# Kernel tuning notes

Measured on AMD Instinct MI355X. Metric: run time of the kernel, lower is better.

The kernel has to match this reference:

```python
import jax, jax.numpy as jnp
import numpy as np

C = 256
DQK = C // 8


def setup_inputs() -> dict:
    key = jax.random.key(0)
    ks = jax.random.split(key, 7)
    B, H, W = 8, 64, 64
    x = jax.random.normal(ks[0], (B, H, W, C), dtype=jnp.float32)
    # 1x1 conv weights (equivalent to per-pixel dense): [Cin, Cout] + bias
    sq = 1.0 / np.sqrt(C)
    Wq = jax.random.normal(ks[1], (C, DQK), dtype=jnp.float32) * sq
    bq = jnp.zeros((DQK,), dtype=jnp.float32)
    Wk = jax.random.normal(ks[2], (C, DQK), dtype=jnp.float32) * sq
    bk = jnp.zeros((DQK,), dtype=jnp.float32)
    Wv = jax.random.normal(ks[3], (C, C), dtype=jnp.float32) * sq
    bv = jnp.zeros((C,), dtype=jnp.float32)
    gamma = jnp.float32(0.5)  # nonzero so attention path affects output/grads
    return {"x": x, "Wq": Wq, "bq": bq, "Wk": Wk, "bk": bk,
            "Wv": Wv, "bv": bv, "gamma": gamma}


def reference(x, Wq, bq, Wk, bk, Wv, bv, gamma):
    B, H, W, c = x.shape
    n = H * W
    xf = x.reshape(B, n, c)                      # [B, hw, C]
    q = xf @ Wq + bq                              # [B, hw, C//8]
    k = xf @ Wk + bk                              # [B, hw, C//8]
    v = xf @ Wv + bv                              # [B, hw, C]
    scores = jnp.einsum('bnd,bmd->bnm', q, k)     # [B, hw, hw], no scaling (faithful)
    attn = jax.nn.softmax(scores, axis=-1)
    out = jnp.einsum('bnm,bmc->bnc', attn, v)     # [B, hw, C]
    out = out.reshape(B, H, W, c)
    return gamma * out + x
```

## Files before the change

kernel.cpp:

```cpp
#include <hip/hip_runtime.h>
#include <math.h>

#define B_ 8
#define N_ 4096
#define C_ 256
#define DQK_ 32

typedef float f32x4  __attribute__((ext_vector_type(4)));
typedef float f32x16 __attribute__((ext_vector_type(16)));
typedef short bf16x8 __attribute__((ext_vector_type(8)));
typedef short bf16x4 __attribute__((ext_vector_type(4)));

__device__ __forceinline__ short f2bf(float f){
  union { float f; unsigned u; } v; v.f = f;
  unsigned r = v.u + 0x7fffu + ((v.u >> 16) & 1u);
  return (short)(r >> 16);
}

__global__ void cast_wt_kernel(const float* __restrict__ Wq, const float* __restrict__ Wk,
                               const float* __restrict__ Wv, short* __restrict__ WT){
  int n = blockIdx.x;
  int k = threadIdx.x;
  float val;
  if (n < 32)       val = Wq[k*32 + n];
  else if (n < 64)  val = Wk[k*32 + (n-32)];
  else              val = Wv[k*256 + (n-64)];
  WT[n*256 + k] = f2bf(val);
}

__global__ __launch_bounds__(256) void proj_kernel(
    const float* __restrict__ x, const short* __restrict__ WT,
    const float* __restrict__ bq, const float* __restrict__ bk, const float* __restrict__ bv,
    short* __restrict__ qws, short* __restrict__ kws, short* __restrict__ vSw){
  __shared__ __align__(16) short sX[64*264];
  __shared__ __align__(16) short sT[64*72];
  int tid = threadIdx.x;
  int lane = tid & 63, wave = tid >> 6;
  int lane15 = lane & 15, quad = lane >> 4;
  int mbase = blockIdx.x * 64;
  int b = mbase >> 12, kvb = mbase & (N_-1);

  const float* xr = x + (size_t)mbase * C_;
  for (int i = 0; i < 8; i++){
    int s = tid + i*256;
    int row = s >> 5, cg = (s & 31) << 3;
    const f32x4* src = (const f32x4*)(xr + row*C_ + cg);
    f32x4 a = src[0], c = src[1];
    bf16x8 p;
    p[0]=f2bf(a[0]); p[1]=f2bf(a[1]); p[2]=f2bf(a[2]); p[3]=f2bf(a[3]);
    p[4]=f2bf(c[0]); p[5]=f2bf(c[1]); p[6]=f2bf(c[2]); p[7]=f2bf(c[3]);
    *(bf16x8*)(sX + row*264 + cg) = p;
  }
  __syncthreads();

  f32x4 acc[5][4];
  for (int i=0;i<5;i++) for (int mt=0;mt<4;mt++) acc[i][mt] = (f32x4)(0.f);

  for (int kc = 0; kc < 8; kc++){
    bf16x8 afr[4];
    #pragma unroll
    for (int mt=0;mt<4;mt++)
      afr[mt] = *(const bf16x8*)(sX + (mt*16+lane15)*264 + kc*32 + quad*8);
    bf16x8 bfr[5];
    #pragma unroll
    for (int i=0;i<5;i++){
      int t = i*4 + wave;
      bfr[i] = *(const bf16x8*)(WT + (size_t)(t*16+lane15)*256 + kc*32 + quad*8);
    }
    #pragma unroll
    for (int i=0;i<5;i++)
      #pragma unroll
      for (int mt=0;mt<4;mt++)
        acc[i][mt] = __builtin_amdgcn_mfma_f32_16x16x32_bf16(afr[mt], bfr[i], acc[i][mt], 0,0,0);
  }

  #pragma unroll
  for (int i=0;i<5;i++){
    int t = i*4 + wave;
    int n0 = t*16 + lane15;
    float bias = (n0 < 32) ? bq[n0] : (n0 < 64 ? bk[n0-32] : bv[n0-64]);
    if (n0 < 64){
      #pragma unroll
      for (int mt=0;mt<4;mt++)
        #pragma unroll
        for (int r=0;r<4;r++)
          sT[(mt*16 + quad*4 + r)*72 + n0] = f2bf(acc[i][mt][r] + bias);
    } else {
      int ch = n0 - 64, cht = ch >> 5, c5 = ch & 31;
      int lanep = c5 | ((quad & 1) << 5);
      int jo = (quad >> 1) * 4;
      #pragma unroll
      for (int mt=0;mt<4;mt++){
        bf16x4 pk;
        pk[0]=f2bf(acc[i][mt][0]+bias); pk[1]=f2bf(acc[i][mt][1]+bias);
        pk[2]=f2bf(acc[i][mt][2]+bias); pk[3]=f2bf(acc[i][mt][3]+bias);
        size_t off = (size_t)b*1048576 + (size_t)(kvb>>6)*16384
                   + (size_t)(mt*8 + cht)*512 + (size_t)lanep*8 + jo;
        *(bf16x4*)(vSw + off) = pk;
      }
    }
  }
  __syncthreads();

  {
    int qt = tid >> 7, p = (tid >> 6) & 1, ln = tid & 63;
    int row = qt*32 + (ln & 31);
    int dcol = p*16 + (ln >> 5)*8;
    bf16x8 vq = *(const bf16x8*)(sT + row*72 + dcol);
    bf16x8 vk = *(const bf16x8*)(sT + row*72 + 32 + dcol);
    size_t qoff = ((((size_t)b*128 + ((kvb>>5) + qt))*2 + p)*64 + ln)*8;
    *(bf16x8*)(qws + qoff) = vq;
    size_t koff = ((size_t)b*64 + (kvb>>6))*2048 + (size_t)((qt*2 + p)*64 + ln)*8;
    *(bf16x8*)(kws + koff) = vk;
  }
}

__global__ __launch_bounds__(256) void flash_kernel(
    const float* __restrict__ x, const short* __restrict__ qws, const short* __restrict__ kws,
    const short* __restrict__ vSw, const float* __restrict__ gptr, float* __restrict__ out){
  __shared__ __align__(16) short sV[2][16384];
  __shared__ __align__(16) short sK[2][2048];
  int tid = threadIdx.x;
  int lane = tid & 63, wave = tid >> 6;
  int l31 = lane & 31, h = lane >> 5;
  int b = blockIdx.x & 7;
  int q0 = (blockIdx.x >> 3) << 7;

  const short* qb = qws + (size_t)b*131072;
  const short* kb = kws + (size_t)b*131072;
  const short* vb = vSw + (size_t)b*1048576;

  int qt = (q0 >> 5) + wave;
  bf16x8 qf0 = *(const bf16x8*)(qb + (size_t)((qt*2+0)*64 + lane)*8);
  bf16x8 qf1 = *(const bf16x8*)(qb + (size_t)((qt*2+1)*64 + lane)*8);

  #pragma unroll
  for (int r=0;r<8;r++)
    __builtin_amdgcn_global_load_lds(
      (const __attribute__((address_space(1))) void*)(vb + r*2048 + tid*8),
      (__attribute__((address_space(3))) void*)(&sV[0][r*2048 + tid*8]), 16, 0, 0);
  __builtin_amdgcn_global_load_lds(
      (const __attribute__((address_space(1))) void*)(kb + tid*8),
      (__attribute__((address_space(3))) void*)(&sK[0][tid*8]), 16, 0, 0);
  __syncthreads();

  f32x16 acc[8], accl;
  #pragma unroll
  for (int t=0;t<8;t++) acc[t] = (f32x16)(0.f);
  accl = (f32x16)(0.f);
  bf16x8 ones;
  #pragma unroll
  for (int j=0;j<8;j++) ones[j] = (short)0x3F80;

  for (int it=0; it<64; it++){
    int cb = it & 1, nb = cb ^ 1;
    if (it < 63){
      const short* vsrc = vb + (size_t)(it+1)*16384;
      #pragma unroll
      for (int r=0;r<8;r++)
        __builtin_amdgcn_global_load_lds(
          (const __attribute__((address_space(1))) void*)(vsrc + r*2048 + tid*8),
          (__attribute__((address_space(3))) void*)(&sV[nb][r*2048 + tid*8]), 16, 0, 0);
      __builtin_amdgcn_global_load_lds(
          (const __attribute__((address_space(1))) void*)(kb + (size_t)(it+1)*2048 + tid*8),
          (__attribute__((address_space(3))) void*)(&sK[nb][tid*8]), 16, 0, 0);
    }

    bf16x8 kf[4];
    #pragma unroll
    for (int f=0;f<4;f++)
      kf[f] = *(const bf16x8*)(&sK[cb][(f*64 + lane)*8]);
    f32x16 s0 = __builtin_amdgcn_mfma_f32_32x32x16_bf16(kf[0], qf0, (f32x16)(0.f), 0,0,0);
    s0        = __builtin_amdgcn_mfma_f32_32x32x16_bf16(kf[1], qf1, s0, 0,0,0);
    f32x16 s1 = __builtin_amdgcn_mfma_f32_32x32x16_bf16(kf[2], qf0, (f32x16)(0.f), 0,0,0);
    s1        = __builtin_amdgcn_mfma_f32_32x32x16_bf16(kf[3], qf1, s1, 0,0,0);

    bf16x8 pf[4];
    #pragma unroll
    for (int j=0;j<8;j++){
      pf[0][j] = f2bf(__expf(s0[j]));
      pf[1][j] = f2bf(__expf(s0[8+j]));
      pf[2][j] = f2bf(__expf(s1[j]));
      pf[3][j] = f2bf(__expf(s1[8+j]));
    }

    #pragma unroll
    for (int kvg=0; kvg<4; kvg++){
      const short* base = &sV[cb][kvg*4096];
      #pragma unroll
      for (int cht=0; cht<8; cht++){
        bf16x8 vf = *(const bf16x8*)(base + (cht*64 + lane)*8);
        acc[cht] = __builtin_amdgcn_mfma_f32_32x32x16_bf16(pf[kvg], vf, acc[cht], 0,0,0);
      }
      accl = __builtin_amdgcn_mfma_f32_32x32x16_bf16(pf[kvg], ones, accl, 0,0,0);
    }
    __syncthreads();
  }

  float g = *gptr;
  const float* xb = x + ((size_t)b*N_ + q0 + wave*32)*C_;
  float*       ob = out + ((size_t)b*N_ + q0 + wave*32)*C_;
  #pragma unroll
  for (int i=0;i<16;i++){
    int q = (i&3) + 8*(i>>2) + 4*h;
    float rv = 1.f / accl[i];
    #pragma unroll
    for (int cht=0; cht<8; cht++){
      int ch = cht*32 + l31;
      ob[(size_t)q*C_ + ch] = g*(acc[cht][i]*rv) + xb[(size_t)q*C_ + ch];
    }
  }
}

extern "C" void kernel_launch(void* const* d_in, const int* in_sizes, int n_in,
                              void* d_out, int out_size, void* d_ws, size_t ws_size,
                              hipStream_t stream){
  const float* x  = (const float*)d_in[0];
  const float* Wq = (const float*)d_in[1];
  const float* bq = (const float*)d_in[2];
  const float* Wk = (const float*)d_in[3];
  const float* bk = (const float*)d_in[4];
  const float* Wv = (const float*)d_in[5];
  const float* bv = (const float*)d_in[6];
  const float* gm = (const float*)d_in[7];
  float* out = (float*)d_out;
  char* ws = (char*)d_ws;
  short* WT  = (short*)ws;
  short* qws = (short*)(ws + 163840);
  short* kws = (short*)(ws + 163840 + 2097152);
  short* vSw = (short*)(ws + 163840 + 2*2097152);

  cast_wt_kernel<<<dim3(320), dim3(256), 0, stream>>>(Wq, Wk, Wv, WT);
  proj_kernel<<<dim3(512), dim3(256), 0, stream>>>(x, WT, bq, bk, bv, qws, kws, vSw);
  flash_kernel<<<dim3(256), dim3(256), 0, stream>>>(x, qws, kws, vSw, gm, out);
}
```

Baseline: 212.9 us.

## Split flash attention work across 8 waves with KV-half split and LDS reduction

```diff
diff --git a/kernel.cpp b/kernel.cpp
--- a/kernel.cpp
+++ b/kernel.cpp
@@ -1,4 +1,5 @@
 #include <hip/hip_runtime.h>
+#include <hip/hip_bf16.h>
 #include <math.h>
 
 #define B_ 8
@@ -115,14 +116,17 @@
   }
 }
 
-__global__ __launch_bounds__(256) void flash_kernel(
+__global__ __launch_bounds__(512, 2) void flash_kernel(
     const float* __restrict__ x, const short* __restrict__ qws, const short* __restrict__ kws,
     const short* __restrict__ vSw, const float* __restrict__ gptr, float* __restrict__ out){
-  __shared__ __align__(16) short sV[2][16384];
-  __shared__ __align__(16) short sK[2][2048];
+  __shared__ __align__(16) char smem[67584];
+  float* Rb  = (float*)smem;
+  float* sLt = (float*)(smem + 65536);
+
   int tid = threadIdx.x;
   int lane = tid & 63, wave = tid >> 6;
   int l31 = lane & 31, h = lane >> 5;
+  int kvh = wave & 1, chh = (wave >> 1) & 1, qh = wave >> 2;
   int b = blockIdx.x & 7;
   int q0 = (blockIdx.x >> 3) << 7;
 
@@ -130,84 +134,149 @@
   const short* kb = kws + (size_t)b*131072;
   const short* vb = vSw + (size_t)b*1048576;
 
-  int qt = (q0 >> 5) + wave;
-  bf16x8 qf0 = *(const bf16x8*)(qb + (size_t)((qt*2+0)*64 + lane)*8);
-  bf16x8 qf1 = *(const bf16x8*)(qb + (size_t)((qt*2+1)*64 + lane)*8);
-
+  int qtg = (q0 >> 5) + qh*2;
+  bf16x8 qf00 = *(const bf16x8*)(qb + (size_t)((qtg*2+0)*64 + lane)*8);
+  bf16x8 qf01 = *(const bf16x8*)(qb + (size_t)((qtg*2+1)*64 + lane)*8);
+  bf16x8 qf10 = *(const bf16x8*)(qb + (size_t)((qtg*2+2)*64 + lane)*8);
+  bf16x8 qf11 = *(const bf16x8*)(qb + (size_t)((qtg*2+3)*64 + lane)*8);
+
+  const short* kf0p = kb + (size_t)((2*kvh+0)*64 + lane)*8;
+  const short* kf1p = kb + (size_t)((2*kvh+1)*64 + lane)*8;
+  bf16x8 kfc0 = *(const bf16x8*)(kf0p);
+  bf16x8 kfc1 = *(const bf16x8*)(kf1p);
+  bf16x8 kfn0 = kfc0, kfn1 = kfc1;
+
+  const short* vb0 = vb + (size_t)(((2*kvh+0)*8 + chh*4)*512 + lane*8);
+  const short* vb1 = vb + (size_t)(((2*kvh+1)*8 + chh*4)*512 + lane*8);
+
+  f32x16 acc0[4], acc1[4];
   #pragma unroll
-  for (int r=0;r<8;r++)
-    __builtin_amdgcn_global_load_lds(
-      (const __attribute__((address_space(1))) void*)(vb + r*2048 + tid*8),
-      (__attribute__((address_space(3))) void*)(&sV[0][r*2048 + tid*8]), 16, 0, 0);
-  __builtin_amdgcn_global_load_lds(
-      (const __attribute__((address_space(1))) void*)(kb + tid*8),
-      (__attribute__((address_space(3))) void*)(&sK[0][tid*8]), 16, 0, 0);
-  __syncthreads();
-
-  f32x16 acc[8], accl;
-  #pragma unroll
-  for (int t=0;t<8;t++) acc[t] = (f32x16)(0.f);
-  accl = (f32x16)(0.f);
-  bf16x8 ones;
-  #pragma unroll
-  for (int j=0;j<8;j++) ones[j] = (short)0x3F80;
+  for (int t=0;t<4;t++){ acc0[t] = (f32x16)(0.f); acc1[t] = (f32x16)(0.f); }
+  float lrow0 = 0.f, lrow1 = 0.f;
 
   for (int it=0; it<64; it++){
-    int cb = it & 1, nb = cb ^ 1;
     if (it < 63){
-      const short* vsrc = vb + (size_t)(it+1)*16384;
+      kfn0 = *(const bf16x8*)(kf0p + (size_t)(it+1)*2048);
+      kfn1 = *(const bf16x8*)(kf1p + (size_t)(it+1)*2048);
+    }
+
+    f32x16 s0 = __builtin_amdgcn_mfma_f32_32x32x16_bf16(kfc0, qf00, (f32x16)(0.f), 0,0,0);
+    s0        = __builtin_amdgcn_mfma_f32_32x32x16_bf16(kfc1, qf01, s0, 0,0,0);
+    f32x16 s1 = __builtin_amdgcn_mfma_f32_32x32x16_bf16(kfc0, qf10, (f32x16)(0.f), 0,0,0);
+    s1        = __builtin_amdgcn_mfma_f32_32x32x16_bf16(kfc1, qf11, s1, 0,0,0);
+
+    bf16x8 pf00, pf01, pf10, pf11;
+    {
+      union { bf16x8 v; unsigned u[4]; } P0, P1, P2, P3;
       #pragma unroll
-      for (int r=0;r<8;r++)
-        __builtin_amdgcn_global_load_lds(
-          (const __attribute__((address_space(1))) void*)(vsrc + r*2048 + tid*8),
-          (__attribute__((address_space(3))) void*)(&sV[nb][r*2048 + tid*8]), 16, 0, 0);
-      __builtin_amdgcn_global_load_lds(
-          (const __attribute__((address_space(1))) void*)(kb + (size_t)(it+1)*2048 + tid*8),
-          (__attribute__((address_space(3))) void*)(&sK[nb][tid*8]), 16, 0, 0);
-    }
-
-    bf16x8 kf[4];
-    #pragma unroll
-    for (int f=0;f<4;f++)
-      kf[f] = *(const bf16x8*)(&sK[cb][(f*64 + lane)*8]);
-    f32x16 s0 = __builtin_amdgcn_mfma_f32_32x32x16_bf16(kf[0], qf0, (f32x16)(0.f), 0,0,0);
-    s0        = __builtin_amdgcn_mfma_f32_32x32x16_bf16(kf[1], qf1, s0, 0,0,0);
-    f32x16 s1 = __builtin_amdgcn_mfma_f32_32x32x16_bf16(kf[2], qf0, (f32x16)(0.f), 0,0,0);
-    s1        = __builtin_amdgcn_mfma_f32_32x32x16_bf16(kf[3], qf1, s1, 0,0,0);
-
-    bf16x8 pf[4];
-    #pragma unroll
-    for (int j=0;j<8;j++){
-      pf[0][j] = f2bf(__expf(s0[j]));
-      pf[1][j] = f2bf(__expf(s0[8+j]));
-      pf[2][j] = f2bf(__expf(s1[j]));
-      pf[3][j] = f2bf(__expf(s1[8+j]));
-    }
-
-    #pragma unroll
-    for (int kvg=0; kvg<4; kvg++){
-      const short* base = &sV[cb][kvg*4096];
-      #pragma unroll
-      for (int cht=0; cht<8; cht++){
-        bf16x8 vf = *(const bf16x8*)(base + (cht*64 + lane)*8);
-        acc[cht] = __builtin_amdgcn_mfma_f32_32x32x16_bf16(pf[kvg], vf, acc[cht], 0,0,0);
+      for (int j=0;j<4;j++){
+        float2 e;
+        e.x = __expf(s0[2*j]);   e.y = __expf(s0[2*j+1]);
+        lrow0 += e.x + e.y;
+        { __hip_bfloat162 t2 = __float22bfloat162_rn(e); __builtin_memcpy(&P0.u[j], &t2, 4); }
+        e.x = __expf(s0[8+2*j]); e.y = __expf(s0[8+2*j+1]);
+        lrow0 += e.x + e.y;
+        { __hip_bfloat162 t2 = __float22bfloat162_rn(e); __builtin_memcpy(&P1.u[j], &t2, 4); }
+        e.x = __expf(s1[2*j]);   e.y = __expf(s1[2*j+1]);
+        lrow1 += e.x + e.y;
+        { __hip_bfloat162 t2 = __float22bfloat162_rn(e); __builtin_memcpy(&P2.u[j], &t2, 4); }
+        e.x = __expf(s1[8+2*j]); e.y = __expf(s1[8+2*j+1]);
+        lrow1 += e.x + e.y;
+        { __hip_bfloat162 t2 = __float22bfloat162_rn(e); __builtin_memcpy(&P3.u[j], &t2, 4); }
       }
-      accl = __builtin_amdgcn_mfma_f32_32x32x16_bf16(pf[kvg], ones, accl, 0,0,0);
-    }
-    __syncthreads();
+      pf00 = P0.v; pf01 = P1.v; pf10 = P2.v; pf11 = P3.v;
+    }
+
+    const short* v0 = vb0 + (size_t)it*16384;
+    const short* v1 = vb1 + (size_t)it*16384;
+    #pragma unroll
+    for (int ct=0; ct<4; ct++){
+      bf16x8 vf = *(const bf16x8*)(v0 + ct*512);
+      acc0[ct] = __builtin_amdgcn_mfma_f32_32x32x16_bf16(pf00, vf, acc0[ct], 0,0,0);
+      acc1[ct] = __builtin_amdgcn_mfma_f32_32x32x16_bf16(pf10, vf, acc1[ct], 0,0,0);
+    }
+    #pragma unroll
+    for (int ct=0; ct<4; ct++){
+      bf16x8 vf = *(const bf16x8*)(v1 + ct*512);
+      acc0[ct] = __builtin_amdgcn_mfma_f32_32x32x16_bf16(pf01, vf, acc0[ct], 0,0,0);
+      acc1[ct] = __builtin_amdgcn_mfma_f32_32x32x16_bf16(pf11, vf, acc1[ct], 0,0,0);
+    }
+    kfc0 = kfn0; kfc1 = kfn1;
+  }
+
+  lrow0 += __shfl_xor(lrow0, 32, 64);
+  lrow1 += __shfl_xor(lrow1, 32, 64);
+  sLt[wave*64 + l31]      = lrow0;
+  sLt[wave*64 + 32 + l31] = lrow1;
+
+  int pw = wave ^ 1;
+  if (kvh == 0){
+    #pragma unroll
+    for (int i=0;i<16;i++){ Rb[wave*2048 + i*64 + lane]        = acc0[2][i];
+                            Rb[wave*2048 + 1024 + i*64 + lane] = acc0[3][i]; }
+  } else {
+    #pragma unroll
+    for (int i=0;i<16;i++){ Rb[wave*2048 + i*64 + lane]        = acc0[0][i];
+                            Rb[wave*2048 + 1024 + i*64 + lane] = acc0[1][i]; }
+  }
+  __syncthreads();
+  if (kvh == 0){
+    #pragma unroll
+    for (int i=0;i<16;i++){ acc0[0][i] += Rb[pw*2048 + i*64 + lane];
+                            acc0[1][i] += Rb[pw*2048 + 1024 + i*64 + lane]; }
+  } else {
+    #pragma unroll
+    for (int i=0;i<16;i++){ acc0[2][i] += Rb[pw*2048 + i*64 + lane];
+                            acc0[3][i] += Rb[pw*2048 + 1024 + i*64 + lane]; }
+  }
+  __syncthreads();
+  if (kvh == 0){
+    #pragma unroll
+    for (int i=0;i<16;i++){ Rb[wave*2048 + i*64 + lane]        = acc1[2][i];
+                            Rb[wave*2048 + 1024 + i*64 + lane] = acc1[3][i]; }
+  } else {
+    #pragma unroll
+    for (int i=0;i<16;i++){ Rb[wave*2048 + i*64 + lane]        = acc1[0][i];
+                            Rb[wave*2048 + 1024 + i*64 + lane] = acc1[1][i]; }
+  }
+  __syncthreads();
+  if (kvh == 0){
+    #pragma unroll
+    for (int i=0;i<16;i++){ acc1[0][i] += Rb[pw*2048 + i*64 + lane];
+                            acc1[1][i] += Rb[pw*2048 + 1024 + i*64 + lane]; }
+  } else {
+    #pragma unroll
+    for (int i=0;i<16;i++){ acc1[2][i] += Rb[pw*2048 + i*64 + lane];
+                            acc1[3][i] += Rb[pw*2048 + 1024 + i*64 + lane]; }
   }
 
   float g = *gptr;
-  const float* xb = x + ((size_t)b*N_ + q0 + wave*32)*C_;
-  float*       ob = out + ((size_t)b*N_ + q0 + wave*32)*C_;
-  #pragma unroll
-  for (int i=0;i<16;i++){
-    int q = (i&3) + 8*(i>>2) + 4*h;
-    float rv = 1.f / accl[i];
-    #pragma unroll
-    for (int cht=0; cht<8; cht++){
-      int ch = cht*32 + l31;
-      ob[(size_t)q*C_ + ch] = g*(acc[cht][i]*rv) + xb[(size_t)q*C_ + ch];
+  int w0 = wave & ~1, w1 = wave | 1;
+  const float* xb = x   + ((size_t)b*N_ + q0 + qh*64)*C_;
+  float*       ob = out + ((size_t)b*N_ + q0 + qh*64)*C_;
+  if (kvh == 0){
+    #pragma unroll
+    for (int i=0;i<16;i++){
+      int qr = (i&3) + 8*(i>>2) + 4*h;
+      float rv0 = 1.f / (sLt[w0*64 + qr]      + sLt[w1*64 + qr]);
+      float rv1 = 1.f / (sLt[w0*64 + 32 + qr] + sLt[w1*64 + 32 + qr]);
+      int ch0 = (chh*4+0)*32 + l31, ch1 = (chh*4+1)*32 + l31;
+      ob[(size_t)qr*C_ + ch0]      = g*(acc0[0][i]*rv0) + xb[(size_t)qr*C_ + ch0];
+      ob[(size_t)qr*C_ + ch1]      = g*(acc0[1][i]*rv0) + xb[(size_t)qr*C_ + ch1];
+      ob[(size_t)(32+qr)*C_ + ch0] = g*(acc1[0][i]*rv1) + xb[(size_t)(32+qr)*C_ + ch0];
+      ob[(size_t)(32+qr)*C_ + ch1] = g*(acc1[1][i]*rv1) + xb[(size_t)(32+qr)*C_ + ch1];
+    }
+  } else {
+    #pragma unroll
+    for (int i=0;i<16;i++){
+      int qr = (i&3) + 8*(i>>2) + 4*h;
+      float rv0 = 1.f / (sLt[w0*64 + qr]      + sLt[w1*64 + qr]);
+      float rv1 = 1.f / (sLt[w0*64 + 32 + qr] + sLt[w1*64 + 32 + qr]);
+      int ch0 = (chh*4+2)*32 + l31, ch1 = (chh*4+3)*32 + l31;
+      ob[(size_t)qr*C_ + ch0]      = g*(acc0[2][i]*rv0) + xb[(size_t)qr*C_ + ch0];
+      ob[(size_t)qr*C_ + ch1]      = g*(acc0[3][i]*rv0) + xb[(size_t)qr*C_ + ch1];
+      ob[(size_t)(32+qr)*C_ + ch0] = g*(acc1[2][i]*rv1) + xb[(size_t)(32+qr)*C_ + ch0];
+      ob[(size_t)(32+qr)*C_ + ch1] = g*(acc1[3][i]*rv1) + xb[(size_t)(32+qr)*C_ + ch1];
     }
   }
 }
@@ -232,5 +301,5 @@
 
   cast_wt_kernel<<<dim3(320), dim3(256), 0, stream>>>(Wq, Wk, Wv, WT);
   proj_kernel<<<dim3(512), dim3(256), 0, stream>>>(x, WT, bq, bk, bv, qws, kws, vSw);
-  flash_kernel<<<dim3(256), dim3(256), 0, stream>>>(x, qws, kws, vSw, gm, out);
-}
+  flash_kernel<<<dim3(256), dim3(512), 0, stream>>>(x, qws, kws, vSw, gm, out);
+}
```

Measured after the change: 197.5 us. -7.2%, faster.
